# Kernel optimization log

Measured on AMD Instinct MI355X. Metric: run time of the kernel, lower is better.

The kernel has to match this reference:

```python
import jax, jax.numpy as jnp
import numpy as np

D = 128          # embed_dim
M = 131072       # merged node states produced at this tree level
K = M // 2       # per-child split between bot-sourced and buf-sourced states
NB = 200000      # size of each source state pool


def setup_inputs() -> dict:
    key = jax.random.key(0)
    ks = jax.random.split(key, 10)
    f32 = jnp.float32
    inp = {
        "h_bot": jax.random.normal(ks[0], (NB, D), dtype=f32),
        "c_bot": jax.random.normal(ks[1], (NB, D), dtype=f32),
        "h_buf": jax.random.normal(ks[2], (NB, D), dtype=f32),
        "c_buf": jax.random.normal(ks[3], (NB, D), dtype=f32),
        # BinaryTreeLSTMCell params: concat([h_l, h_r]) -> 5 gates (i, o, u, f_l, f_r)
        "W": jax.random.normal(ks[4], (2 * D, 5 * D), dtype=f32) / np.sqrt(2 * D).astype(np.float32),
        "b": jnp.zeros((5 * D,), dtype=f32),
        # child 0 (left): first K slots filled from bot, rest from buf
        "bot_froms0": jax.random.randint(ks[5], (K,), 0, NB, dtype=jnp.int32),
        "bot_tos0": jnp.arange(K, dtype=jnp.int32),
        "prev_froms0": jax.random.randint(ks[6], (K,), 0, NB, dtype=jnp.int32),
        "prev_tos0": jnp.arange(K, M, dtype=jnp.int32),
        # child 1 (right): opposite partition
        "bot_froms1": jax.random.randint(ks[7], (K,), 0, NB, dtype=jnp.int32),
        "bot_tos1": jnp.arange(K, M, dtype=jnp.int32),
        "prev_froms1": jax.random.randint(ks[8], (K,), 0, NB, dtype=jnp.int32),
        "prev_tos1": jnp.arange(K, dtype=jnp.int32),
    }
    return inp


def _multi_index_select(src_bot, src_buf, bot_froms, bot_tos, prev_froms, prev_tos):
    # Gather rows from two source pools and scatter them into aligned slots [M, D].
    out = jnp.zeros((M, src_bot.shape[1]), dtype=src_bot.dtype)
    out = out.at[bot_tos].set(src_bot[bot_froms])
    out = out.at[prev_tos].set(src_buf[prev_froms])
    return out


def _binary_tree_lstm(h_l, c_l, h_r, c_r, W, b):
    gates = jnp.concatenate([h_l, h_r], axis=1) @ W + b  # [M, 5D]
    i, o, u, f_l, f_r = jnp.split(gates, 5, axis=1)
    i, o = jax.nn.sigmoid(i), jax.nn.sigmoid(o)
    f_l, f_r = jax.nn.sigmoid(f_l), jax.nn.sigmoid(f_r)
    u = jnp.tanh(u)
    c = i * u + f_l * c_l + f_r * c_r
    h = o * jnp.tanh(c)
    return h, c


def reference(h_bot, c_bot, h_buf, c_buf, W, b,
              bot_froms0, bot_tos0, prev_froms0, prev_tos0,
              bot_froms1, bot_tos1, prev_froms1, prev_tos1):
    # batch_tree_lstm2: per-child gather/scatter state selection + binary TreeLSTM merge
    h_l = _multi_index_select(h_bot, h_buf, bot_froms0, bot_tos0, prev_froms0, prev_tos0)
    c_l = _multi_index_select(c_bot, c_buf, bot_froms0, bot_tos0, prev_froms0, prev_tos0)
    h_r = _multi_index_select(h_bot, h_buf, bot_froms1, bot_tos1, prev_froms1, prev_tos1)
    c_r = _multi_index_select(c_bot, c_buf, bot_froms1, bot_tos1, prev_froms1, prev_tos1)
    return _binary_tree_lstm(h_l, c_l, h_r, c_r, W, b)
```

## Files before the change

### kernel.cpp

```cpp
#include <hip/hip_runtime.h>
#include <hip/hip_bf16.h>
#include <stdint.h>

#define AS1 __attribute__((address_space(1)))
#define AS3 __attribute__((address_space(3)))

typedef __attribute__((ext_vector_type(8))) short bf16x8;
typedef __attribute__((ext_vector_type(4))) short short4v;
typedef __attribute__((ext_vector_type(4))) float f32x4;

static constexpr int D = 128;
static constexpr int M = 131072;
static constexpr int KHALF = 65536;
static constexpr int FIVE_D = 640;
static constexpr int FLAGBIT = 1 << 30;
static constexpr int IDXMASK = FLAGBIT - 1;

__device__ __forceinline__ void gl_lds16(const void* g, void* l) {
  __builtin_amdgcn_global_load_lds((const AS1 void*)g, (AS3 void*)l, 16, 0, 0);
}

__device__ __forceinline__ short f2bf(float x) {
  __hip_bfloat16 h = __float2bfloat16(x);
  return (short)__bfloat16_as_ushort(h);
}

__global__ void build_tables(const int* __restrict__ bf0, const int* __restrict__ bt0,
                             const int* __restrict__ pf0, const int* __restrict__ pt0,
                             const int* __restrict__ bf1, const int* __restrict__ bt1,
                             const int* __restrict__ pf1, const int* __restrict__ pt1,
                             int* __restrict__ tabL, int* __restrict__ tabR) {
  int j = blockIdx.x * blockDim.x + threadIdx.x;
  if (j < KHALF) {
    tabL[bt0[j]] = bf0[j];
    tabL[pt0[j]] = pf0[j] | FLAGBIT;
    tabR[bt1[j]] = bf1[j];
    tabR[pt1[j]] = pf1[j] | FLAGBIT;
  }
}

__global__ void pack_w(const float* __restrict__ W, unsigned short* __restrict__ P) {
  int idx = blockIdx.x * blockDim.x + threadIdx.x;
  int c = idx / (FIVE_D * 32);
  int rem = idx - c * (FIVE_D * 32);
  int n = rem >> 5;
  int kk = rem & 31;
  P[idx] = __bfloat16_as_ushort(__float2bfloat16(W[(c * 32 + kk) * FIVE_D + n]));
}

__global__ __launch_bounds__(512, 4) void tree_lstm_fused(
    const float* __restrict__ h_bot, const float* __restrict__ c_bot,
    const float* __restrict__ h_buf, const float* __restrict__ c_buf,
    const unsigned short* __restrict__ Wp, const float* __restrict__ bias,
    const int* __restrict__ tabL, const int* __restrict__ tabR,
    float* __restrict__ out) {
  __shared__ __align__(16) short A_lds[64 * 32];
  __shared__ __align__(16) short W_lds[FIVE_D * 32];

  const int tid = threadIdx.x;
  const int lane = tid & 63;
  const int wv = tid >> 6;
  const int quad = lane >> 4;
  const int l16 = lane & 15;
  const int m_base = blockIdx.x * 64;

  f32x4 acc[4][5];
  const f32x4 zero = {0.f, 0.f, 0.f, 0.f};
#pragma unroll
  for (int mt = 0; mt < 4; ++mt)
#pragma unroll
    for (int g = 0; g < 5; ++g) acc[mt][g] = zero;

  const int a_row = tid >> 3;
  const int a_seg = tid & 7;
  const int mA = m_base + a_row;
  const int sLa = tabL[mA];
  const int sRa = tabR[mA];
  const float* pL = ((sLa & FLAGBIT) ? h_buf : h_bot) + (size_t)(sLa & IDXMASK) * D + a_seg * 4;
  const float* pR = ((sRa & FLAGBIT) ? h_buf : h_bot) + (size_t)(sRa & IDXMASK) * D + a_seg * 4;

#pragma unroll 1
  for (int c = 0; c < 8; ++c) {
    if (c) __syncthreads();
    const unsigned short* wsrc = Wp + c * (FIVE_D * 32);
#pragma unroll
    for (int i = 0; i < 5; ++i) {
      const int off = (i * 512 + tid) * 8;
      gl_lds16(wsrc + off, &W_lds[off]);
    }
    const float* asrc = (c < 4) ? (pL + c * 32) : (pR + (c - 4) * 32);
    const float4 av = *(const float4*)asrc;
    short4v bv;
    bv.x = f2bf(av.x);
    bv.y = f2bf(av.y);
    bv.z = f2bf(av.z);
    bv.w = f2bf(av.w);
    *(short4v*)&A_lds[tid * 4] = bv;
    __syncthreads();

    bf16x8 afrag[4];
#pragma unroll
    for (int mt = 0; mt < 4; ++mt)
      afrag[mt] = *(const bf16x8*)&A_lds[(mt * 16 + l16) * 32 + 8 * quad];
#pragma unroll
    for (int g = 0; g < 5; ++g) {
      const bf16x8 bfrag = *(const bf16x8*)&W_lds[(g * 128 + wv * 16 + l16) * 32 + 8 * quad];
#pragma unroll
      for (int mt = 0; mt < 4; ++mt)
        acc[mt][g] = __builtin_amdgcn_mfma_f32_16x16x32_bf16(afrag[mt], bfrag, acc[mt][g], 0, 0, 0);
    }
  }

  const int d = wv * 16 + l16;
  const float bi = bias[0 * D + d];
  const float bo = bias[1 * D + d];
  const float bu = bias[2 * D + d];
  const float bl = bias[3 * D + d];
  const float br = bias[4 * D + d];
  float* outh = out;
  float* outc = out + (size_t)M * D;

#pragma unroll
  for (int mt = 0; mt < 4; ++mt) {
#pragma unroll
    for (int r = 0; r < 4; ++r) {
      const int m = m_base + mt * 16 + quad * 4 + r;
      const int sL = tabL[m];
      const int sR = tabR[m];
      const float* clp = (sL & FLAGBIT) ? c_buf : c_bot;
      const float* crp = (sR & FLAGBIT) ? c_buf : c_bot;
      const float cl = clp[(size_t)(sL & IDXMASK) * D + d];
      const float cr = crp[(size_t)(sR & IDXMASK) * D + d];
      const float gi = acc[mt][0][r] + bi;
      const float go = acc[mt][1][r] + bo;
      const float gu = acc[mt][2][r] + bu;
      const float gfl = acc[mt][3][r] + bl;
      const float gfr = acc[mt][4][r] + br;
      const float iv = 1.f / (1.f + __expf(-gi));
      const float ov = 1.f / (1.f + __expf(-go));
      const float uv = 2.f / (1.f + __expf(-2.f * gu)) - 1.f;
      const float flv = 1.f / (1.f + __expf(-gfl));
      const float frv = 1.f / (1.f + __expf(-gfr));
      const float cc = iv * uv + flv * cl + frv * cr;
      const float hh = ov * (2.f / (1.f + __expf(-2.f * cc)) - 1.f);
      outh[(size_t)m * D + d] = hh;
      outc[(size_t)m * D + d] = cc;
    }
  }
}

extern "C" void kernel_launch(void* const* d_in, const int* in_sizes, int n_in,
                              void* d_out, int out_size, void* d_ws, size_t ws_size,
                              hipStream_t stream) {
  const float* h_bot = (const float*)d_in[0];
  const float* c_bot = (const float*)d_in[1];
  const float* h_buf = (const float*)d_in[2];
  const float* c_buf = (const float*)d_in[3];
  const float* W = (const float*)d_in[4];
  const float* b = (const float*)d_in[5];
  const int* bf0 = (const int*)d_in[6];
  const int* bt0 = (const int*)d_in[7];
  const int* pf0 = (const int*)d_in[8];
  const int* pt0 = (const int*)d_in[9];
  const int* bf1 = (const int*)d_in[10];
  const int* bt1 = (const int*)d_in[11];
  const int* pf1 = (const int*)d_in[12];
  const int* pt1 = (const int*)d_in[13];

  int* tabL = (int*)d_ws;
  int* tabR = tabL + M;
  unsigned short* Wp = (unsigned short*)(tabR + M);

  hipLaunchKernelGGL(build_tables, dim3(KHALF / 256), dim3(256), 0, stream,
                     bf0, bt0, pf0, pt0, bf1, bt1, pf1, pt1, tabL, tabR);
  hipLaunchKernelGGL(pack_w, dim3((8 * FIVE_D * 32) / 256), dim3(256), 0, stream, W, Wp);
  hipLaunchKernelGGL(tree_lstm_fused, dim3(M / 64), dim3(512), 0, stream,
                     h_bot, c_bot, h_buf, c_buf, Wp, b, tabL, tabR, (float*)d_out);
}
```

Measured before the change: 452.7 us.

## Stage full A tile in LDS once and read W fragments directly from global

New measurement: 496.7 us. 1.1x slower.

```diff
diff --git a/kernel.cpp b/kernel.cpp
--- a/kernel.cpp
+++ b/kernel.cpp
@@ -2,11 +2,7 @@
 #include <hip/hip_bf16.h>
 #include <stdint.h>
 
-#define AS1 __attribute__((address_space(1)))
-#define AS3 __attribute__((address_space(3)))
-
 typedef __attribute__((ext_vector_type(8))) short bf16x8;
-typedef __attribute__((ext_vector_type(4))) short short4v;
 typedef __attribute__((ext_vector_type(4))) float f32x4;
 
 static constexpr int D = 128;
@@ -15,10 +11,6 @@
 static constexpr int FIVE_D = 640;
 static constexpr int FLAGBIT = 1 << 30;
 static constexpr int IDXMASK = FLAGBIT - 1;
-
-__device__ __forceinline__ void gl_lds16(const void* g, void* l) {
-  __builtin_amdgcn_global_load_lds((const AS1 void*)g, (AS3 void*)l, 16, 0, 0);
-}
 
 __device__ __forceinline__ short f2bf(float x) {
   __hip_bfloat16 h = __float2bfloat16(x);
@@ -54,8 +46,7 @@
     const unsigned short* __restrict__ Wp, const float* __restrict__ bias,
     const int* __restrict__ tabL, const int* __restrict__ tabR,
     float* __restrict__ out) {
-  __shared__ __align__(16) short A_lds[64 * 32];
-  __shared__ __align__(16) short W_lds[FIVE_D * 32];
+  __shared__ __align__(16) short A_lds[64 * 256];
 
   const int tid = threadIdx.x;
   const int lane = tid & 63;
@@ -64,6 +55,32 @@
   const int l16 = lane & 15;
   const int m_base = blockIdx.x * 64;
 
+  {
+    const int row = tid >> 3;
+    const int gs0 = (tid & 7) * 4;
+    const int mA = m_base + row;
+    const int s = (gs0 < 16) ? tabL[mA] : tabR[mA];
+    const float* src = ((s & FLAGBIT) ? h_buf : h_bot) + (size_t)(s & IDXMASK) * D
+                     + (gs0 * 8 & 127);
+    float4 v[8];
+#pragma unroll
+    for (int i = 0; i < 8; ++i) v[i] = ((const float4*)src)[i];
+#pragma unroll
+    for (int j = 0; j < 4; ++j) {
+      bf16x8 g;
+      g[0] = f2bf(v[2 * j].x);
+      g[1] = f2bf(v[2 * j].y);
+      g[2] = f2bf(v[2 * j].z);
+      g[3] = f2bf(v[2 * j].w);
+      g[4] = f2bf(v[2 * j + 1].x);
+      g[5] = f2bf(v[2 * j + 1].y);
+      g[6] = f2bf(v[2 * j + 1].z);
+      g[7] = f2bf(v[2 * j + 1].w);
+      *(bf16x8*)&A_lds[((gs0 + j) * 64 + row) * 8] = g;
+    }
+  }
+  __syncthreads();
+
   f32x4 acc[4][5];
   const f32x4 zero = {0.f, 0.f, 0.f, 0.f};
 #pragma unroll
@@ -71,43 +88,21 @@
 #pragma unroll
     for (int g = 0; g < 5; ++g) acc[mt][g] = zero;
 
-  const int a_row = tid >> 3;
-  const int a_seg = tid & 7;
-  const int mA = m_base + a_row;
-  const int sLa = tabL[mA];
-  const int sRa = tabR[mA];
-  const float* pL = ((sLa & FLAGBIT) ? h_buf : h_bot) + (size_t)(sLa & IDXMASK) * D + a_seg * 4;
-  const float* pR = ((sRa & FLAGBIT) ? h_buf : h_bot) + (size_t)(sRa & IDXMASK) * D + a_seg * 4;
+  const short* a_ptr = &A_lds[(quad * 64 + l16) * 8];
+  const unsigned short* b_ptr = Wp + (wv * 512 + l16 * 32 + quad * 8);
 
-#pragma unroll 1
+#pragma unroll
   for (int c = 0; c < 8; ++c) {
-    if (c) __syncthreads();
-    const unsigned short* wsrc = Wp + c * (FIVE_D * 32);
-#pragma unroll
-    for (int i = 0; i < 5; ++i) {
-      const int off = (i * 512 + tid) * 8;
-      gl_lds16(wsrc + off, &W_lds[off]);
-    }
-    const float* asrc = (c < 4) ? (pL + c * 32) : (pR + (c - 4) * 32);
-    const float4 av = *(const float4*)asrc;
-    short4v bv;
-    bv.x = f2bf(av.x);
-    bv.y = f2bf(av.y);
-    bv.z = f2bf(av.z);
-    bv.w = f2bf(av.w);
-    *(short4v*)&A_lds[tid * 4] = bv;
-    __syncthreads();
-
-    bf16x8 afrag[4];
+    bf16x8 af[4];
 #pragma unroll
     for (int mt = 0; mt < 4; ++mt)
-      afrag[mt] = *(const bf16x8*)&A_lds[(mt * 16 + l16) * 32 + 8 * quad];
+      af[mt] = *(const bf16x8*)(a_ptr + c * 2048 + mt * 128);
 #pragma unroll
     for (int g = 0; g < 5; ++g) {
-      const bf16x8 bfrag = *(const bf16x8*)&W_lds[(g * 128 + wv * 16 + l16) * 32 + 8 * quad];
+      const bf16x8 bf_ = *(const bf16x8*)(b_ptr + c * 20480 + g * 4096);
 #pragma unroll
       for (int mt = 0; mt < 4; ++mt)
-        acc[mt][g] = __builtin_amdgcn_mfma_f32_16x16x32_bf16(afrag[mt], bfrag, acc[mt][g], 0, 0, 0);
+        acc[mt][g] = __builtin_amdgcn_mfma_f32_16x16x32_bf16(af[mt], bf_, acc[mt][g], 0, 0, 0);
     }
   }
 
@@ -122,15 +117,18 @@
 
 #pragma unroll
   for (int mt = 0; mt < 4; ++mt) {
+    float cl[4], cr[4];
 #pragma unroll
     for (int r = 0; r < 4; ++r) {
       const int m = m_base + mt * 16 + quad * 4 + r;
       const int sL = tabL[m];
       const int sR = tabR[m];
-      const float* clp = (sL & FLAGBIT) ? c_buf : c_bot;
-      const float* crp = (sR & FLAGBIT) ? c_buf : c_bot;
-      const float cl = clp[(size_t)(sL & IDXMASK) * D + d];
-      const float cr = crp[(size_t)(sR & IDXMASK) * D + d];
+      cl[r] = (((sL & FLAGBIT) ? c_buf : c_bot) + (size_t)(sL & IDXMASK) * D)[d];
+      cr[r] = (((sR & FLAGBIT) ? c_buf : c_bot) + (size_t)(sR & IDXMASK) * D)[d];
+    }
+#pragma unroll
+    for (int r = 0; r < 4; ++r) {
+      const int m = m_base + mt * 16 + quad * 4 + r;
       const float gi = acc[mt][0][r] + bi;
       const float go = acc[mt][1][r] + bo;
       const float gu = acc[mt][2][r] + bu;
@@ -141,10 +139,10 @@
       const float uv = 2.f / (1.f + __expf(-2.f * gu)) - 1.f;
       const float flv = 1.f / (1.f + __expf(-gfl));
       const float frv = 1.f / (1.f + __expf(-gfr));
-      const float cc = iv * uv + flv * cl + frv * cr;
+      const float cc = iv * uv + flv * cl[r] + frv * cr[r];
       const float hh = ov * (2.f / (1.f + __expf(-2.f * cc)) - 1.f);
-      outh[(size_t)m * D + d] = hh;
-      outc[(size_t)m * D + d] = cc;
+      __builtin_nontemporal_store(hh, &outh[(size_t)m * D + d]);
+      __builtin_nontemporal_store(cc, &outc[(size_t)m * D + d]);
     }
   }
 }
```
